# Kernel tuning notes

Hardware: AMD Instinct MI355X
Metric: run time of the kernel (lower is better)

Reference implementation:

```python
import jax, jax.numpy as jnp
import numpy as np

BLOCK_SIZE = 32
BLOCK_COUNTS = 4
NEG = -1e9
SEQ_LENS = np.array([512, 384, 448, 256], dtype=np.int64)


def setup_inputs():
    key = jax.random.key(0)
    ks = jax.random.split(key, 5)
    T = int(SEQ_LENS.sum()); H = 4; D = 64
    offs = np.concatenate([[0], np.cumsum(SEQ_LENS)]).astype(np.int64)
    return {
        "q": jax.random.normal(ks[0], (T, H, D), jnp.float32),
        "k": jax.random.normal(ks[1], (T, H, D), jnp.float32),
        "v": jax.random.normal(ks[2], (T, H, D), jnp.float32),
        "g_cmp": jax.random.uniform(ks[3], (T, H), jnp.float32),
        "g_slc": jax.random.uniform(ks[4], (T, H), jnp.float32),
        "x_offsets": jnp.asarray(offs),
    }


def _silu(x):
    return x * jax.nn.sigmoid(x)


def _forward(q, k, v, g_cmp, g_slc, offs):
    bs = BLOCK_SIZE
    B = len(offs) - 1
    seq_lens = offs[1:] - offs[:-1]              # np [B]
    T, H, D = q.shape
    max_n = int(seq_lens.max())
    nb = (max_n + bs - 1) // bs                  # max compressed blocks
    L = nb * bs                                  # padded length (multiple of bs)
    batch_ids = np.repeat(np.arange(B), seq_lens)
    local_ids = np.arange(T) - offs[:-1][batch_ids]

    def pad(x):  # jagged [T, ...] -> padded [B, L, ...]
        return jnp.zeros((B, L) + x.shape[1:], x.dtype).at[batch_ids, local_ids].set(x)

    pq, pk, pv = pad(q), pad(k), pad(v)
    # block-pooled (mean) compressed K/V; partial blocks also divided by bs, as in torch
    k_cmp = pk.reshape(B, nb, bs, H, D).sum(axis=2) / bs   # [B, nb, H, D]
    v_cmp = pv.reshape(B, nb, bs, H, D).sum(axis=2) / bs

    scale = D ** -0.5
    pos = np.arange(max_n)                       # local query positions
    qblk = pos // bs
    blk = np.arange(nb)
    causal = qblk[:, None] >= blk[None, :]       # [max_n, nb]
    seq_valid = pos[None, :] < seq_lens[:, None]  # [B, max_n]
    cmp_lens = (seq_lens + bs - 1) // bs
    blk_valid = blk[None, :] < cmp_lens[:, None]  # [B, nb]

    pq_m = pq[:, :max_n]                          # [B, max_n, H, D]
    scores = jnp.einsum('bqhd,bkhd->bhqk', pq_m, k_cmp) * scale  # [B,H,max_n,nb]

    # --- compressed branch: mask to -1e9, SiLU, zero masked (matches cmp kernel) ---
    m_full = (jnp.asarray(causal)[None, None]
              & jnp.asarray(seq_valid)[:, None, :, None]
              & jnp.asarray(blk_valid)[:, None, None, :])
    m_zero = jnp.asarray(causal)[None, None] & jnp.asarray(blk_valid)[:, None, None, :]
    p_cmp = jnp.where(m_zero, _silu(jnp.where(m_full, scores, NEG)), 0.0)
    o_cmp_pad = jnp.einsum('bhqk,bkhd->bqhd', p_cmp, v_cmp)
    o_cmp_pad = o_cmp_pad * pad(g_cmp)[:, :max_n, :, None]
    o_cmp = o_cmp_pad[batch_ids, local_ids]       # back to jagged [T,H,D]

    # --- per-token top-S block selection on causally masked compressed scores ---
    sel_scores = jnp.where(jnp.asarray(causal)[None, None], scores, -jnp.inf)
    S = min(BLOCK_COUNTS, nb)
    _, topk = jax.lax.top_k(sel_scores, S)        # [B,H,max_n,S] block ids

    # --- selected branch: gather raw K/V from the chosen blocks ---
    r = np.arange(bs)
    tpos = topk[..., None] * bs + r               # [B,H,max_n,S,bs] local key pos < L
    pk_h = pk.transpose(0, 2, 1, 3)               # [B,H,L,D]
    pv_h = pv.transpose(0, 2, 1, 3)
    idx = tpos.reshape(B, H, -1)
    k_sel = jnp.take_along_axis(pk_h, idx[..., None], axis=2).reshape(B, H, max_n, S, bs, D)
    v_sel = jnp.take_along_axis(pv_h, idx[..., None], axis=2).reshape(B, H, max_n, S, bs, D)
    pq_h = pq_m.transpose(0, 2, 1, 3)             # [B,H,max_n,D]
    s_slc = jnp.einsum('bhmd,bhmsrd->bhmsr', pq_h, k_sel) * scale
    within = tpos < jnp.asarray(seq_lens)[:, None, None, None, None]
    caus = tpos <= jnp.asarray(pos)[None, None, :, None, None]
    p_slc = jnp.where(within & caus, _silu(s_slc), 0.0)
    o_slc_pad = jnp.einsum('bhmsr,bhmsrd->bmhd', p_slc, v_sel)
    o_slc_pad = o_slc_pad * pad(g_slc)[:, :max_n, :, None]
    o_slc = o_slc_pad[batch_ids, local_ids]
    return o_cmp, o_slc


def reference(q, k, v, g_cmp, g_slc, x_offsets):
    return _forward(q, k, v, g_cmp, g_slc, np.asarray(x_offsets))
```

## Files before the change

kernel.cpp:

```cpp
#include <hip/hip_runtime.h>
#include <hip/hip_bf16.h>
#include <math.h>

#define HH 4
#define DD 64
#define BS 32
#define SSEL 4
#define STRIDE (HH * DD)

typedef __attribute__((ext_vector_type(8))) short bf16x8;
typedef __attribute__((ext_vector_type(4))) float f32x4;

__device__ __forceinline__ float silu_f(float x) { return x / (1.0f + __expf(-x)); }

__device__ __forceinline__ unsigned int pk2bf(float a, float b) {
    union { __hip_bfloat16 h[2]; unsigned int u; } cu;
    cu.h[0] = __float2bfloat16(a);
    cu.h[1] = __float2bfloat16(b);
    return cu.u;
}

__global__ __launch_bounds__(256) void nsa_compress(
        const float* __restrict__ kin, const float* __restrict__ vin,
        const int* __restrict__ offs, int B, int nbcap,
        float* __restrict__ kc, float* __restrict__ vc) {
    int wid  = (blockIdx.x * blockDim.x + threadIdx.x) >> 6;
    int lane = threadIdx.x & 63;
    if (wid >= B * nbcap * HH * 2) return;
    int kind = wid & 1;
    int rest = wid >> 1;
    int h    = rest % HH;
    int blk  = (rest / HH) % nbcap;
    int b    = rest / (HH * nbcap);
    int off  = offs[b];
    int n    = offs[b + 1] - off;
    int ncmp = (n + BS - 1) / BS;
    if (blk >= ncmp) return;
    int cbase = 0;
    for (int i = 0; i < b; ++i) cbase += (offs[i + 1] - offs[i] + BS - 1) / BS;

    int rg = lane >> 4, d16 = lane & 15;
    const float* src = kind ? vin : kin;
    const float4* sp = (const float4*)(src + (size_t)(off + blk * BS) * STRIDE + h * DD + d16 * 4);
    int rmax = min(BS, n - blk * BS);
    float4 acc = {0.f, 0.f, 0.f, 0.f};
    #pragma unroll
    for (int i = 0; i < 8; ++i) {
        int row = rg * 8 + i;
        if (row < rmax) {
            float4 x = sp[(size_t)row * (STRIDE / 4)];
            acc.x += x.x; acc.y += x.y; acc.z += x.z; acc.w += x.w;
        }
    }
    #pragma unroll
    for (int m = 16; m <= 32; m <<= 1) {
        acc.x += __shfl_xor(acc.x, m, 64);
        acc.y += __shfl_xor(acc.y, m, 64);
        acc.z += __shfl_xor(acc.z, m, 64);
        acc.w += __shfl_xor(acc.w, m, 64);
    }
    if (rg == 0) {
        float4 r;
        r.x = acc.x * (1.f / BS); r.y = acc.y * (1.f / BS);
        r.z = acc.z * (1.f / BS); r.w = acc.w * (1.f / BS);
        float* dst = (kind ? vc : kc) + ((size_t)(cbase + blk) * HH + h) * DD + d16 * 4;
        *(float4*)dst = r;
    }
}

__global__ __launch_bounds__(512, 2) void nsa_fused(
        const float* __restrict__ q, const float* __restrict__ k,
        const float* __restrict__ v, const float* __restrict__ gc,
        const float* __restrict__ gs, const int* __restrict__ offs,
        const float* __restrict__ kc, const float* __restrict__ vc,
        int B, int T, float* __restrict__ out) {
    __shared__ float Qf[32][68];
    __shared__ float Kc[16][68];
    __shared__ float Vc[16][64];
    __shared__ float Sc[32][17];
    __shared__ float Ps[32][17];
    __shared__ unsigned char selb[32][16];
    __shared__ unsigned int  Msk[32];
    __shared__ unsigned short Qs[32][64];
    __shared__ __align__(16) char UN[4 * 32 * 68 * 4];

    unsigned int (*Pw)[32][20] = (unsigned int (*)[32][20])UN;
    float        (*Op)[32][68] = (float (*)[32][68])UN;

    int qbh = blockIdx.x;
    int h   = qbh & (HH - 1);
    int qb  = qbh / HH;

    int b = -1, lb = 0, cum = 0, off = 0, n = 0;
    for (int i = 0; i < B; ++i) {
        int o0 = offs[i], o1 = offs[i + 1];
        int nbi = (o1 - o0 + BS - 1) / BS;
        if (qb < cum + nbi) { b = i; lb = qb - cum; off = o0; n = o1 - o0; break; }
        cum += nbi;
    }
    if (b < 0) return;
    int cbase = cum;
    int t0  = off + lb * BS;
    int nbl = lb + 1;
    const float scale = 0.125f;
    int tid = threadIdx.x;
    int w = tid >> 6, lane = tid & 63;
    int l15 = lane & 15, g = lane >> 4;

    {
        int row = tid >> 4, dg = tid & 15;
        int trow = min(t0 + row, T - 1);
        float4 a = *(const float4*)(q + (size_t)trow * STRIDE + h * DD + dg * 4);
        a.x *= scale; a.y *= scale; a.z *= scale; a.w *= scale;
        *(float4*)&Qf[row][dg * 4] = a;
        uint2 uu = { pk2bf(a.x, a.y), pk2bf(a.z, a.w) };
        *(uint2*)&Qs[row][(((dg >> 1) ^ (row & 7)) * 8) + (dg & 1) * 4] = uu;
    }

    for (int idx = tid; idx < nbl * 16; idx += 512) {
        int row = idx >> 4, dg = idx & 15;
        size_t src = ((size_t)(cbase + row) * HH + h) * DD + dg * 4;
        *(float4*)&Kc[row][dg * 4] = *(const float4*)(kc + src);
        *(float4*)&Vc[row][dg * 4] = *(const float4*)(vc + src);
    }
    __syncthreads();

    {
        int qq = tid >> 4, j = tid & 15;
        if (j < nbl) {
            float s = 0.f;
            #pragma unroll
            for (int i = 0; i < 16; ++i) {
                float4 qv = *(float4*)&Qf[qq][i * 4];
                float4 kk = *(float4*)&Kc[j][i * 4];
                s += qv.x * kk.x + qv.y * kk.y + qv.z * kk.z + qv.w * kk.w;
            }
            Sc[qq][j] = s;
        }
    }
    __syncthreads();

    {
        int qq = tid >> 4, j = tid & 15;
        if (j < nbl) {
            float sj = Sc[qq][j];
            int rank = 0;
            for (int i = 0; i < nbl; ++i) {
                float si = Sc[qq][i];
                rank += (si > sj) || (si == sj && i < j);
            }
            selb[qq][j] = (unsigned char)(rank < SSEL);
            Ps[qq][j]   = silu_f(sj);
        } else {
            selb[qq][j] = 0;
        }
    }
    __syncthreads();

    if (tid < 32) {
        unsigned int m = 0;
        #pragma unroll
        for (int j = 0; j < 16; ++j) m |= ((unsigned int)selb[tid][j]) << j;
        Msk[tid] = m;
    }
    {
        int qq = tid >> 4, dg = tid & 15;
        float4 o = {0.f, 0.f, 0.f, 0.f};
        for (int blk = 0; blk < nbl; ++blk) {
            float p = Ps[qq][blk];
            float4 vv = *(float4*)&Vc[blk][dg * 4];
            o.x += p * vv.x; o.y += p * vv.y; o.z += p * vv.z; o.w += p * vv.w;
        }
        if (lb * BS + qq < n) {
            float gv = gc[(size_t)(t0 + qq) * HH + h];
            o.x *= gv; o.y *= gv; o.z *= gv; o.w *= gv;
            *(float4*)(out + (size_t)(t0 + qq) * STRIDE + h * DD + dg * 4) = o;
        }
    }
    __syncthreads();

    unsigned int Msq[2];
    Msq[0] = Msk[l15];
    Msq[1] = Msk[16 + l15];

    f32x4 oacc[4][2];
    #pragma unroll
    for (int dt = 0; dt < 4; ++dt)
        #pragma unroll
        for (int qt = 0; qt < 2; ++qt)
            oacc[dt][qt] = (f32x4){0.f, 0.f, 0.f, 0.f};

    #pragma unroll 1
    for (int kb = w; kb <= lb; kb += 8) {
        const float* kbase = k + (size_t)(off + kb * BS) * STRIDE + h * DD;
        const float* vbase = v + (size_t)(off + kb * BS) * STRIDE + h * DD;

        float4 kf[2][2][2];
        #pragma unroll
        for (int tt = 0; tt < 2; ++tt)
            #pragma unroll
            for (int ds = 0; ds < 2; ++ds) {
                const float4* p = (const float4*)(kbase + (size_t)(tt * 16 + l15) * STRIDE
                                                  + ds * 32 + g * 8);
                kf[tt][ds][0] = p[0];
                kf[tt][ds][1] = p[1];
            }
        float tv[4][8];
        #pragma unroll
        for (int dt = 0; dt < 4; ++dt)
            #pragma unroll
            for (int j = 0; j < 8; ++j)
                tv[dt][j] = vbase[(size_t)(g * 8 + j) * STRIDE + dt * 16 + l15];

        bf16x8 a1[2][2];
        #pragma unroll
        for (int tt = 0; tt < 2; ++tt)
            #pragma unroll
            for (int ds = 0; ds < 2; ++ds) {
                union { unsigned int u[4]; bf16x8 v8; } cu;
                float4 x = kf[tt][ds][0], y = kf[tt][ds][1];
                cu.u[0] = pk2bf(x.x, x.y); cu.u[1] = pk2bf(x.z, x.w);
                cu.u[2] = pk2bf(y.x, y.y); cu.u[3] = pk2bf(y.z, y.w);
                a1[tt][ds] = cu.v8;
            }
        bf16x8 b1[2][2];
        #pragma unroll
        for (int ds = 0; ds < 2; ++ds)
            #pragma unroll
            for (int tt = 0; tt < 2; ++tt)
                b1[tt][ds] = *(bf16x8*)&Qs[tt * 16 + l15][((g + ds * 4) ^ (l15 & 7)) * 8];

        f32x4 s[2][2];
        #pragma unroll
        for (int kt = 0; kt < 2; ++kt)
            #pragma unroll
            for (int qt = 0; qt < 2; ++qt) {
                s[kt][qt] = (f32x4){0.f, 0.f, 0.f, 0.f};
                s[kt][qt] = __builtin_amdgcn_mfma_f32_16x16x32_bf16(a1[kt][0], b1[qt][0], s[kt][qt], 0, 0, 0);
                s[kt][qt] = __builtin_amdgcn_mfma_f32_16x16x32_bf16(a1[kt][1], b1[qt][1], s[kt][qt], 0, 0, 0);
            }

        #pragma unroll
        for (int kt = 0; kt < 2; ++kt)
            #pragma unroll
            for (int qt = 0; qt < 2; ++qt) {
                bool selbit = (Msq[qt] >> kb) & 1u;
                float pv[4];
                #pragma unroll
                for (int r = 0; r < 4; ++r) {
                    int k_l = kt * 16 + g * 4 + r;
                    int q_l = qt * 16 + l15;
                    bool ok = selbit && (kb < lb || k_l <= q_l);
                    pv[r] = ok ? silu_f(s[kt][qt][r]) : 0.f;
                }
                Pw[w][qt * 16 + l15][kt * 8 + g * 2 + 0] = pk2bf(pv[0], pv[1]);
                Pw[w][qt * 16 + l15][kt * 8 + g * 2 + 1] = pk2bf(pv[2], pv[3]);
            }
        bf16x8 b2[2];
        b2[0] = *(bf16x8*)&Pw[w][l15][g * 4];
        b2[1] = *(bf16x8*)&Pw[w][16 + l15][g * 4];

        bf16x8 a2[4];
        #pragma unroll
        for (int dt = 0; dt < 4; ++dt) {
            union { unsigned int u[4]; bf16x8 v8; } cu;
            cu.u[0] = pk2bf(tv[dt][0], tv[dt][1]);
            cu.u[1] = pk2bf(tv[dt][2], tv[dt][3]);
            cu.u[2] = pk2bf(tv[dt][4], tv[dt][5]);
            cu.u[3] = pk2bf(tv[dt][6], tv[dt][7]);
            a2[dt] = cu.v8;
        }

        #pragma unroll
        for (int dt = 0; dt < 4; ++dt)
            #pragma unroll
            for (int qt = 0; qt < 2; ++qt)
                oacc[dt][qt] = __builtin_amdgcn_mfma_f32_16x16x32_bf16(a2[dt], b2[qt], oacc[dt][qt], 0, 0, 0);
    }
    __syncthreads();

    if (w < 4) {
        #pragma unroll
        for (int dt = 0; dt < 4; ++dt)
            #pragma unroll
            for (int qt = 0; qt < 2; ++qt)
                #pragma unroll
                for (int r = 0; r < 4; ++r)
                    Op[w][qt * 16 + l15][dt * 16 + g * 4 + r] = oacc[dt][qt][r];
    }
    __syncthreads();
    if (w >= 4) {
        #pragma unroll
        for (int dt = 0; dt < 4; ++dt)
            #pragma unroll
            for (int qt = 0; qt < 2; ++qt)
                #pragma unroll
                for (int r = 0; r < 4; ++r)
                    Op[w - 4][qt * 16 + l15][dt * 16 + g * 4 + r] += oacc[dt][qt][r];
    }
    __syncthreads();

    {
        int qq = tid >> 4, dg = tid & 15;
        if (lb * BS + qq < n) {
            float gv = gs[(size_t)(t0 + qq) * HH + h];
            float o[4];
            #pragma unroll
            for (int i = 0; i < 4; ++i) {
                int d = dg * 4 + i;
                o[i] = (Op[0][qq][d] + Op[1][qq][d] + Op[2][qq][d] + Op[3][qq][d]) * gv;
            }
            *(float4*)(out + (size_t)T * STRIDE + (size_t)(t0 + qq) * STRIDE + h * DD + dg * 4)
                = (float4){o[0], o[1], o[2], o[3]};
        }
    }
}

extern "C" void kernel_launch(void* const* d_in, const int* in_sizes, int n_in,
                              void* d_out, int out_size, void* d_ws, size_t ws_size,
                              hipStream_t stream) {
    const float* q    = (const float*)d_in[0];
    const float* k    = (const float*)d_in[1];
    const float* v    = (const float*)d_in[2];
    const float* gc   = (const float*)d_in[3];
    const float* gs   = (const float*)d_in[4];
    const int*   offs = (const int*)d_in[5];

    int B = in_sizes[5] - 1;
    int T = out_size / (2 * STRIDE);
    int nbcap  = (T + BS - 1) / BS;
    int nqbcap = nbcap + B;

    size_t cmp_elems = (size_t)(nbcap + B) * STRIDE;
    float* kc = (float*)d_ws;
    float* vc = kc + cmp_elems;

    int waves1 = B * nbcap * HH * 2;
    nsa_compress<<<dim3((unsigned)((waves1 * 64 + 255) / 256)), dim3(256), 0, stream>>>(
        k, v, offs, B, nbcap, kc, vc);

    nsa_fused<<<dim3((unsigned)(nqbcap * HH)), dim3(512), 0, stream>>>(
        q, k, v, gc, gs, offs, kc, vc, B, T, (float*)d_out);
}
```

Measured before the change: 20.40 us.

## Merge compress and fused attention kernels into one cooperative launch with grid sync

Drops the separate block-pooling compress kernel and folds that work into the start of the fused attention kernel. The pooling is spread over all waves of the grid, then a cooperative-groups grid sync runs before the attention phase. This removes one kernel launch and the gap between the two kernels. In exchange it needs a cooperative launch, which limits the grid to what fits on the device at once, and it adds the cost of a grid-wide barrier.

```diff
diff --git a/kernel.cpp b/kernel.cpp
--- a/kernel.cpp
+++ b/kernel.cpp
@@ -1,6 +1,9 @@
 #include <hip/hip_runtime.h>
 #include <hip/hip_bf16.h>
+#include <hip/hip_cooperative_groups.h>
 #include <math.h>
+
+namespace cg = cooperative_groups;
 
 #define HH 4
 #define DD 64
@@ -20,59 +23,11 @@
     return cu.u;
 }
 
-__global__ __launch_bounds__(256) void nsa_compress(
-        const float* __restrict__ kin, const float* __restrict__ vin,
-        const int* __restrict__ offs, int B, int nbcap,
-        float* __restrict__ kc, float* __restrict__ vc) {
-    int wid  = (blockIdx.x * blockDim.x + threadIdx.x) >> 6;
-    int lane = threadIdx.x & 63;
-    if (wid >= B * nbcap * HH * 2) return;
-    int kind = wid & 1;
-    int rest = wid >> 1;
-    int h    = rest % HH;
-    int blk  = (rest / HH) % nbcap;
-    int b    = rest / (HH * nbcap);
-    int off  = offs[b];
-    int n    = offs[b + 1] - off;
-    int ncmp = (n + BS - 1) / BS;
-    if (blk >= ncmp) return;
-    int cbase = 0;
-    for (int i = 0; i < b; ++i) cbase += (offs[i + 1] - offs[i] + BS - 1) / BS;
-
-    int rg = lane >> 4, d16 = lane & 15;
-    const float* src = kind ? vin : kin;
-    const float4* sp = (const float4*)(src + (size_t)(off + blk * BS) * STRIDE + h * DD + d16 * 4);
-    int rmax = min(BS, n - blk * BS);
-    float4 acc = {0.f, 0.f, 0.f, 0.f};
-    #pragma unroll
-    for (int i = 0; i < 8; ++i) {
-        int row = rg * 8 + i;
-        if (row < rmax) {
-            float4 x = sp[(size_t)row * (STRIDE / 4)];
-            acc.x += x.x; acc.y += x.y; acc.z += x.z; acc.w += x.w;
-        }
-    }
-    #pragma unroll
-    for (int m = 16; m <= 32; m <<= 1) {
-        acc.x += __shfl_xor(acc.x, m, 64);
-        acc.y += __shfl_xor(acc.y, m, 64);
-        acc.z += __shfl_xor(acc.z, m, 64);
-        acc.w += __shfl_xor(acc.w, m, 64);
-    }
-    if (rg == 0) {
-        float4 r;
-        r.x = acc.x * (1.f / BS); r.y = acc.y * (1.f / BS);
-        r.z = acc.z * (1.f / BS); r.w = acc.w * (1.f / BS);
-        float* dst = (kind ? vc : kc) + ((size_t)(cbase + blk) * HH + h) * DD + d16 * 4;
-        *(float4*)dst = r;
-    }
-}
-
-__global__ __launch_bounds__(512, 2) void nsa_fused(
+__global__ __launch_bounds__(512, 2) void nsa_coop(
         const float* __restrict__ q, const float* __restrict__ k,
         const float* __restrict__ v, const float* __restrict__ gc,
         const float* __restrict__ gs, const int* __restrict__ offs,
-        const float* __restrict__ kc, const float* __restrict__ vc,
+        float* __restrict__ kc, float* __restrict__ vc,
         int B, int T, float* __restrict__ out) {
     __shared__ float Qf[32][68];
     __shared__ float Kc[16][68];
@@ -87,6 +42,62 @@
     unsigned int (*Pw)[32][20] = (unsigned int (*)[32][20])UN;
     float        (*Op)[32][68] = (float (*)[32][68])UN;
 
+    int tid = threadIdx.x;
+    int w = tid >> 6, lane = tid & 63;
+    int l15 = lane & 15, g = lane >> 4;
+    const float scale = 0.125f;
+
+    {
+        int tcb = 0;
+        #pragma unroll 1
+        for (int i = 0; i < B; ++i) tcb += (offs[i + 1] - offs[i] + BS - 1) / BS;
+        int totalUnits = tcb * HH * 2;
+        int nwg = (int)gridDim.x;
+        #pragma unroll 1
+        for (int u = w * nwg + (int)blockIdx.x; u < totalUnits; u += 8 * nwg) {
+            int ci = u / (HH * 2), rest = u % (HH * 2);
+            int h2 = rest >> 1, kind = rest & 1;
+            int bb = 0, c0 = 0;
+            #pragma unroll 1
+            for (;;) {
+                int nc = (offs[bb + 1] - offs[bb] + BS - 1) / BS;
+                if (ci < c0 + nc) break;
+                c0 += nc; ++bb;
+            }
+            int blk  = ci - c0;
+            int off2 = offs[bb];
+            int nn   = offs[bb + 1] - off2;
+            int rg = lane >> 4, d16 = lane & 15;
+            const float* src = kind ? v : k;
+            const float4* sp = (const float4*)(src + (size_t)(off2 + blk * BS) * STRIDE
+                                               + h2 * DD + d16 * 4);
+            int rmax = min(BS, nn - blk * BS);
+            float4 acc = {0.f, 0.f, 0.f, 0.f};
+            #pragma unroll
+            for (int i = 0; i < 8; ++i) {
+                int row = rg * 8 + i;
+                if (row < rmax) {
+                    float4 x = sp[(size_t)row * (STRIDE / 4)];
+                    acc.x += x.x; acc.y += x.y; acc.z += x.z; acc.w += x.w;
+                }
+            }
+            #pragma unroll
+            for (int m = 16; m <= 32; m <<= 1) {
+                acc.x += __shfl_xor(acc.x, m, 64);
+                acc.y += __shfl_xor(acc.y, m, 64);
+                acc.z += __shfl_xor(acc.z, m, 64);
+                acc.w += __shfl_xor(acc.w, m, 64);
+            }
+            if (rg == 0) {
+                float4 r;
+                r.x = acc.x * (1.f / BS); r.y = acc.y * (1.f / BS);
+                r.z = acc.z * (1.f / BS); r.w = acc.w * (1.f / BS);
+                *(float4*)((kind ? vc : kc) + ((size_t)ci * HH + h2) * DD + d16 * 4) = r;
+            }
+        }
+    }
+    cg::this_grid().sync();
+
     int qbh = blockIdx.x;
     int h   = qbh & (HH - 1);
     int qb  = qbh / HH;
@@ -102,10 +113,6 @@
     int cbase = cum;
     int t0  = off + lb * BS;
     int nbl = lb + 1;
-    const float scale = 0.125f;
-    int tid = threadIdx.x;
-    int w = tid >> 6, lane = tid & 63;
-    int l15 = lane & 15, g = lane >> 4;
 
     {
         int row = tid >> 4, dg = tid & 15;
@@ -116,7 +123,6 @@
         uint2 uu = { pk2bf(a.x, a.y), pk2bf(a.z, a.w) };
         *(uint2*)&Qs[row][(((dg >> 1) ^ (row & 7)) * 8) + (dg & 1) * 4] = uu;
     }
-
     for (int idx = tid; idx < nbl * 16; idx += 512) {
         int row = idx >> 4, dg = idx & 15;
         size_t src = ((size_t)(cbase + row) * HH + h) * DD + dg * 4;
@@ -334,11 +340,12 @@
     size_t cmp_elems = (size_t)(nbcap + B) * STRIDE;
     float* kc = (float*)d_ws;
     float* vc = kc + cmp_elems;
-
-    int waves1 = B * nbcap * HH * 2;
-    nsa_compress<<<dim3((unsigned)((waves1 * 64 + 255) / 256)), dim3(256), 0, stream>>>(
-        k, v, offs, B, nbcap, kc, vc);
-
-    nsa_fused<<<dim3((unsigned)(nqbcap * HH)), dim3(512), 0, stream>>>(
-        q, k, v, gc, gs, offs, kc, vc, B, T, (float*)d_out);
+    float* outp = (float*)d_out;
+
+    int G = nqbcap * HH;
+    void* kargs[] = { (void*)&q, (void*)&k, (void*)&v, (void*)&gc, (void*)&gs,
+                      (void*)&offs, (void*)&kc, (void*)&vc,
+                      (void*)&B, (void*)&T, (void*)&outp };
+    hipLaunchCooperativeKernel((const void*)nsa_coop, dim3((unsigned)G), dim3(512),
+                               kargs, 0, stream);
 }
```

Result: slower. 50.93 us (+149.6%).
